# Kernel optimization log

Measured on AMD Instinct MI355X. Metric: run time of the kernel, lower is better.

## Reference

```python
import jax, jax.numpy as jnp
import numpy as np

B, S, D = 64, 196, 768           # batch, num_tokens, dim
E, K = 4, 2                      # num experts (MoM internal default), top-k routing
TH = int(S * 1.0)                # token-mixing hidden (hidden_ratio=1.0)
MH = int(D * 4.0)                # channel MLP hidden (mlp_ratio=4.0)
EPS = 1e-6


def _ln(x, g, b):
    mu = jnp.mean(x, axis=-1, keepdims=True)
    var = jnp.mean((x - mu) ** 2, axis=-1, keepdims=True)
    return (x - mu) / jnp.sqrt(var + EPS) * g + b


def setup_inputs() -> dict:
    key = jax.random.key(0)
    ks = jax.random.split(key, 8)
    w = lambda k, sh: jax.random.normal(k, sh, dtype=jnp.float32) * 0.02
    return {
        "x": jax.random.normal(ks[0], (B, S, D), dtype=jnp.float32),
        "gamma1": jnp.ones((D,), jnp.float32), "beta1": jnp.zeros((D,), jnp.float32),
        "Wg": w(ks[1], (D, E)), "bg": jnp.zeros((E,), jnp.float32),
        "W1": w(ks[2], (E, S, TH)), "b1": jnp.zeros((E, TH), jnp.float32),
        "W2": w(ks[3], (E, TH, S)), "b2": jnp.zeros((E, S), jnp.float32),
        "gamma2": jnp.ones((D,), jnp.float32), "beta2": jnp.zeros((D,), jnp.float32),
        "Wm1": w(ks[4], (D, MH)), "bm1": jnp.zeros((MH,), jnp.float32),
        "Wm2": w(ks[5], (MH, D)), "bm2": jnp.zeros((D,), jnp.float32),
    }


def reference(x, gamma1, beta1, Wg, bg, W1, b1, W2, b2,
              gamma2, beta2, Wm1, bm1, Wm2, bm2):
    # --- pre-norm 1 + MoM token mixer ---
    normed = _ln(x, gamma1, beta1)                               # [B,S,D]
    logits = jnp.mean(normed, axis=1) @ Wg + bg                  # [B,E] per-sample router
    probs = jax.nn.softmax(logits, axis=-1)
    topv, topi = jax.lax.top_k(probs, K)                         # [B,K]
    topv = topv / jnp.sum(topv, axis=-1, keepdims=True)          # renormalize top-k
    combine = jnp.zeros((B, E), probs.dtype).at[jnp.arange(B)[:, None], topi].set(topv)
    xt = jnp.transpose(normed, (0, 2, 1))                        # [B,D,S] mix over tokens
    h = jax.nn.gelu(jnp.einsum('bds,esh->bedh', xt, W1) + b1[None, :, None, :],
                    approximate=False)                           # [B,E,D,TH]
    o = jnp.einsum('bedh,ehs->beds', h, W2) + b2[None, :, None, :]  # [B,E,D,S]
    mom_out = jnp.einsum('be,beds->bsd', combine, o)             # [B,S,D]
    x1 = x + mom_out
    # --- pre-norm 2 + channel MLP ---
    n2 = _ln(x1, gamma2, beta2)
    mlp = jax.nn.gelu(n2 @ Wm1 + bm1, approximate=False) @ Wm2 + bm2
    out = x1 + mlp
    # --- Switch-style load-balancing aux loss ---
    mask = (combine > 0).astype(probs.dtype)                     # [B,E]
    aux_loss = E * jnp.sum(jnp.mean(mask, axis=0) * jnp.mean(probs, axis=0))
    return out, aux_loss
```

## Files before the change

### kernel.cpp

```cpp
#include <hip/hip_runtime.h>
#include <hip/hip_bf16.h>
#include <math.h>

#define BB 64
#define SS 196
#define DD 768
#define EE 4
#define KKE 2
#define THH 196
#define MHH 3072
#define N1 (BB*SS*DD)
#define MM (BB*SS)
#define PP 256

typedef __bf16 bf16x8 __attribute__((ext_vector_type(8)));
typedef float f32x4 __attribute__((ext_vector_type(4)));

__device__ __forceinline__ float gelu_act(float x){
    float y = 1.5957691216057308f*(x + 0.044715f*x*x*x);
    float e = __expf(y);
    float t = 1.f - 2.f/(e+1.f);
    return 0.5f*x*(1.f+t);
}

__global__ __launch_bounds__(256) void ln_bf16_kernel(const float* __restrict__ x,
                                                      const float* __restrict__ g,
                                                      const float* __restrict__ b,
                                                      __hip_bfloat16* __restrict__ out,
                                                      float* __restrict__ muo,
                                                      float* __restrict__ rso){
    int row = blockIdx.x;
    int tid = threadIdx.x;
    const float* xr = x + (size_t)row * DD;
    float v0 = xr[tid], v1 = xr[tid+256], v2 = xr[tid+512];
    float s = v0+v1+v2, ss = v0*v0+v1*v1+v2*v2;
    __shared__ float sh[10];
    int lane = tid & 63, wid = tid >> 6;
    #pragma unroll
    for (int o=32;o>0;o>>=1){ s += __shfl_down(s,o); ss += __shfl_down(ss,o); }
    if (lane==0){ sh[wid]=s; sh[4+wid]=ss; }
    __syncthreads();
    if (tid==0){
        float S1=sh[0]+sh[1]+sh[2]+sh[3], S2=sh[4]+sh[5]+sh[6]+sh[7];
        float mu = S1/DD; float var = S2/DD - mu*mu;
        float rs = rsqrtf(var + 1e-6f);
        sh[8]=mu; sh[9]=rs;
        muo[row]=mu; rso[row]=rs;
    }
    __syncthreads();
    float mu=sh[8], rs=sh[9];
    __hip_bfloat16* orow = out + (size_t)row*DD;
    orow[tid]     = __float2bfloat16((v0-mu)*rs*g[tid]     + b[tid]);
    orow[tid+256] = __float2bfloat16((v1-mu)*rs*g[tid+256] + b[tid+256]);
    orow[tid+512] = __float2bfloat16((v2-mu)*rs*g[tid+512] + b[tid+512]);
}

__global__ __launch_bounds__(256) void transpose_bf16_kernel(const float* __restrict__ src,
                                                             __hip_bfloat16* __restrict__ dst,
                                                             int R, int C){
    __shared__ float t[32][33];
    int c0 = blockIdx.x*32, r0 = blockIdx.y*32;
    int tx = threadIdx.x & 31, ty = threadIdx.x >> 5;
    #pragma unroll
    for (int rr = ty; rr < 32; rr += 8)
        t[rr][tx] = src[(size_t)(r0+rr)*C + c0 + tx];
    __syncthreads();
    #pragma unroll
    for (int cc = ty; cc < 32; cc += 8)
        dst[(size_t)(c0+cc)*R + r0 + tx] = __float2bfloat16(t[tx][cc]);
}

__global__ __launch_bounds__(256) void transpose_pad_w_kernel(const float* __restrict__ src0,
                                                              __hip_bfloat16* __restrict__ dst0,
                                                              int R, int C){
    const float* src = src0 + (size_t)blockIdx.z*R*C;
    __hip_bfloat16* dst = dst0 + (size_t)blockIdx.z*PP*PP;
    __shared__ float t[32][33];
    int c0 = blockIdx.x*32, r0 = blockIdx.y*32;
    int tx = threadIdx.x & 31, ty = threadIdx.x >> 5;
    #pragma unroll
    for (int rr = ty; rr < 32; rr += 8)
        t[rr][tx] = (r0+rr < R && c0+tx < C) ? src[(size_t)(r0+rr)*C + c0 + tx] : 0.f;
    __syncthreads();
    #pragma unroll
    for (int cc = ty; cc < 32; cc += 8)
        dst[(size_t)(c0+cc)*PP + r0 + tx] = __float2bfloat16(t[tx][cc]);
}

__global__ __launch_bounds__(256) void transpose_pad_n_kernel(const __hip_bfloat16* __restrict__ src,
                                                              __hip_bfloat16* __restrict__ dst){
    int b = blockIdx.z;
    __shared__ __hip_bfloat16 t[64][66];
    int d0 = blockIdx.x*64, s0 = blockIdx.y*64;
    int lane = threadIdx.x & 63, q = threadIdx.x >> 6;
    for (int i=q; i<64; i+=4){
        int s = s0+i;
        t[i][lane] = (s < SS) ? src[((size_t)b*SS + s)*DD + d0 + lane]
                              : __float2bfloat16(0.f);
    }
    __syncthreads();
    for (int i=q; i<64; i+=4){
        int d = d0+i;
        dst[((size_t)b*DD + d)*PP + s0 + lane] = t[lane][i];
    }
}

__global__ __launch_bounds__(384) void meanvec_kernel(const float* __restrict__ x,
                                                      const float* __restrict__ mu,
                                                      const float* __restrict__ rs,
                                                      const float* __restrict__ g1,
                                                      const float* __restrict__ b1,
                                                      float* __restrict__ mv){
    int b = blockIdx.y, d = blockIdx.x*384 + threadIdx.x;
    __shared__ float smu[SS], srs[SS];
    for (int s=threadIdx.x; s<SS; s+=384){ smu[s]=mu[b*SS+s]; srs[s]=rs[b*SS+s]; }
    __syncthreads();
    const float* base = x + (size_t)b*SS*DD + d;
    float a0=0.f, a1=0.f;
    for (int s=0;s<SS;s+=2){
        a0 += (base[(size_t)s*DD]     - smu[s])  * srs[s];
        a1 += (base[(size_t)(s+1)*DD] - smu[s+1])* srs[s+1];
    }
    mv[(size_t)b*DD + d] = g1[d]*((a0+a1)/(float)SS) + b1[d];
}

__global__ __launch_bounds__(64) void logits_kernel(const float* __restrict__ mv,
                                                    const float* __restrict__ Wg,
                                                    const float* __restrict__ bg,
                                                    float* __restrict__ combine,
                                                    float* __restrict__ probs,
                                                    int* __restrict__ topi,
                                                    float* __restrict__ topw){
    int b = blockIdx.x, lane = threadIdx.x;
    float pl[EE] = {0.f,0.f,0.f,0.f};
    #pragma unroll
    for (int i=0;i<DD/64;++i){
        int d = lane + i*64;
        float m = mv[(size_t)b*DD + d];
        #pragma unroll
        for (int e=0;e<EE;++e) pl[e] += m * Wg[d*EE + e];
    }
    #pragma unroll
    for (int e=0;e<EE;++e){
        #pragma unroll
        for (int o=32;o>0;o>>=1) pl[e] += __shfl_down(pl[e], o);
    }
    if (lane==0){
        float lg[EE];
        for (int e=0;e<EE;++e) lg[e] = pl[e] + bg[e];
        float mx = lg[0];
        for (int e=1;e<EE;++e) mx = fmaxf(mx, lg[e]);
        float p[EE]; float sum=0.f;
        for (int e=0;e<EE;++e){ p[e]=expf(lg[e]-mx); sum+=p[e]; }
        for (int e=0;e<EE;++e) p[e] /= sum;
        int i0=0; for (int e=1;e<EE;++e) if (p[e]>p[i0]) i0=e;
        int i1=-1;
        for (int e=0;e<EE;++e){ if (e==i0) continue; if (i1<0 || p[e]>p[i1]) i1=e; }
        float v0=p[i0], v1=p[i1], rsum=v0+v1;
        float w0=v0/rsum, w1=v1/rsum;
        for (int e=0;e<EE;++e){ probs[b*EE+e]=p[e]; combine[b*EE+e]=0.f; }
        combine[b*EE+i0]=w0; combine[b*EE+i1]=w1;
        topi[b*KKE]=i0; topi[b*KKE+1]=i1;
        topw[b*KKE]=w0; topw[b*KKE+1]=w1;
    }
}

__global__ __launch_bounds__(256) void aux_kernel(const float* __restrict__ combine,
                                                  const float* __restrict__ probs,
                                                  float* __restrict__ aux_out){
    int tid = threadIdx.x; int e = tid>>6, b = tid&63;
    float m = combine[b*EE+e] > 0.f ? 1.f : 0.f;
    float p = probs[b*EE+e];
    #pragma unroll
    for (int o=32;o>0;o>>=1){ m += __shfl_down(m,o); p += __shfl_down(p,o); }
    __shared__ float sh[EE];
    if ((tid&63)==0) sh[e] = (m/(float)BB)*(p/(float)BB);
    __syncthreads();
    if (tid==0) aux_out[0] = (float)EE * (sh[0]+sh[1]+sh[2]+sh[3]);
}

__global__ __launch_bounds__(256) void tok_gemm1_kernel(
    const __hip_bfloat16* __restrict__ nTp,
    const __hip_bfloat16* __restrict__ w1tp,
    const float* __restrict__ b1,
    const int* __restrict__ topi,
    __hip_bfloat16* __restrict__ htok)
{
    __shared__ __hip_bfloat16 smem[128*64*2];
    __hip_bfloat16* As = smem;
    __hip_bfloat16* Bs = smem + 128*64;
    int tid=threadIdx.x, lane=tid&63, w=tid>>6;
    int wm=w>>1, wn=w&1, l15=lane&15, l4=lane>>4;
    int be = blockIdx.z, b = be>>1;
    int e = __builtin_amdgcn_readfirstlane(topi[b*KKE + (be&1)]);
    int m0 = blockIdx.y*128, n0 = blockIdx.x*128;
    const __hip_bfloat16* A  = nTp  + ((size_t)b*DD + m0)*PP;
    const __hip_bfloat16* Bt = w1tp + ((size_t)e*PP + n0)*PP;
    f32x4 acc[4][4];
    #pragma unroll
    for (int mi=0;mi<4;++mi)
        #pragma unroll
        for (int ni=0;ni<4;++ni) acc[mi][ni] = (f32x4){0.f,0.f,0.f,0.f};

    int srow = w*32 + (lane>>3), sc = lane&7;
    int soff = srow*64 + ((sc ^ (srow&7))<<3);
    const __hip_bfloat16* Ap = A + (size_t)srow*PP + sc*8;
    const __hip_bfloat16* Bp = Bt + (size_t)srow*PP + sc*8;
    bf16x8 va[4], vb[4];
    #pragma unroll
    for (int i=0;i<4;++i){
        va[i] = *reinterpret_cast<const bf16x8*>(Ap + (size_t)i*8*PP);
        vb[i] = *reinterpret_cast<const bf16x8*>(Bp + (size_t)i*8*PP);
    }
    for (int k0=0; k0<PP; k0+=64){
        __syncthreads();
        #pragma unroll
        for (int i=0;i<4;++i){
            *reinterpret_cast<bf16x8*>(&As[soff + i*8*64]) = va[i];
            *reinterpret_cast<bf16x8*>(&Bs[soff + i*8*64]) = vb[i];
        }
        __syncthreads();
        if (k0+64 < PP){
            #pragma unroll
            for (int i=0;i<4;++i){
                va[i] = *reinterpret_cast<const bf16x8*>(Ap + (size_t)i*8*PP + (k0+64));
                vb[i] = *reinterpret_cast<const bf16x8*>(Bp + (size_t)i*8*PP + (k0+64));
            }
        }
        #pragma unroll
        for (int kk=0;kk<2;++kk){
            bf16x8 af[4], bfr[4];
            #pragma unroll
            for (int mi=0;mi<4;++mi){
                int r = wm*64 + mi*16 + l15, kc = kk*4 + l4;
                af[mi] = *reinterpret_cast<const bf16x8*>(&As[r*64 + ((kc ^ (r&7))<<3)]);
            }
            #pragma unroll
            for (int ni=0;ni<4;++ni){
                int r = wn*64 + ni*16 + l15, kc = kk*4 + l4;
                bfr[ni] = *reinterpret_cast<const bf16x8*>(&Bs[r*64 + ((kc ^ (r&7))<<3)]);
            }
            #pragma unroll
            for (int mi=0;mi<4;++mi)
                #pragma unroll
                for (int ni=0;ni<4;++ni)
                    acc[mi][ni] = __builtin_amdgcn_mfma_f32_16x16x32_bf16(af[mi], bfr[ni], acc[mi][ni], 0, 0, 0);
        }
    }
    __syncthreads();
    __hip_bfloat16* Ht = smem;
    #pragma unroll
    for (int mi=0;mi<4;++mi){
        #pragma unroll
        for (int ni=0;ni<4;++ni){
            int colL = wn*64 + ni*16 + l15;
            int col = n0 + colL;
            float bv = (col < THH) ? b1[e*THH + col] : 0.f;
            #pragma unroll
            for (int r=0;r<4;++r){
                int rowL = wm*64 + mi*16 + l4*4 + r;
                float v = (col < THH) ? gelu_act(acc[mi][ni][r] + bv) : 0.f;
                Ht[rowL*128 + colL] = __float2bfloat16(v);
            }
        }
    }
    __syncthreads();
    for (int i = tid; i < 128*128/8; i += 256){
        int rowL = i >> 4, c8 = i & 15;
        *reinterpret_cast<bf16x8*>(&htok[((size_t)be*DD + m0 + rowL)*PP + n0 + c8*8])
            = *reinterpret_cast<const bf16x8*>(&Ht[rowL*128 + c8*8]);
    }
}

__global__ __launch_bounds__(256) void tok_gemm2_kernel(
    const __hip_bfloat16* __restrict__ htok,
    const __hip_bfloat16* __restrict__ w2tp,
    const float* __restrict__ b2,
    const int* __restrict__ topi, const float* __restrict__ topw,
    const float* __restrict__ x, float* __restrict__ x1)
{
    __shared__ __hip_bfloat16 As[128*64];
    __shared__ __hip_bfloat16 Bs[128*64];
    int tid=threadIdx.x, lane=tid&63, w=tid>>6;
    int wm=w>>1, wn=w&1, l15=lane&15, l4=lane>>4;
    int b = blockIdx.z;
    int m0 = blockIdx.y*128, n0 = blockIdx.x*128;
    float w0 = topw[b*KKE], w1 = topw[b*KKE+1];
    f32x4 acc[4][4];
    #pragma unroll
    for (int mi=0;mi<4;++mi)
        #pragma unroll
        for (int ni=0;ni<4;++ni) acc[mi][ni] = (f32x4){0.f,0.f,0.f,0.f};

    int srow = w*32 + (lane>>3), sc = lane&7;
    int soff = srow*64 + ((sc ^ (srow&7))<<3);

    for (int pass=0; pass<2; ++pass){
        int e = __builtin_amdgcn_readfirstlane(topi[b*KKE + pass]);
        const __hip_bfloat16* Ap = htok + ((size_t)(b*KKE+pass)*DD + m0 + srow)*PP + sc*8;
        const __hip_bfloat16* Bp = w2tp + ((size_t)e*PP + n0 + srow)*PP + sc*8;
        bf16x8 va[4], vb[4];
        #pragma unroll
        for (int i=0;i<4;++i){
            va[i] = *reinterpret_cast<const bf16x8*>(Ap + (size_t)i*8*PP);
            vb[i] = *reinterpret_cast<const bf16x8*>(Bp + (size_t)i*8*PP);
        }
        for (int k0=0; k0<PP; k0+=64){
            __syncthreads();
            #pragma unroll
            for (int i=0;i<4;++i){
                *reinterpret_cast<bf16x8*>(&As[soff + i*8*64]) = va[i];
                *reinterpret_cast<bf16x8*>(&Bs[soff + i*8*64]) = vb[i];
            }
            __syncthreads();
            if (k0+64 < PP){
                #pragma unroll
                for (int i=0;i<4;++i){
                    va[i] = *reinterpret_cast<const bf16x8*>(Ap + (size_t)i*8*PP + (k0+64));
                    vb[i] = *reinterpret_cast<const bf16x8*>(Bp + (size_t)i*8*PP + (k0+64));
                }
            }
            #pragma unroll
            for (int kk=0;kk<2;++kk){
                bf16x8 af[4], bfr[4];
                #pragma unroll
                for (int mi=0;mi<4;++mi){
                    int r = wm*64 + mi*16 + l15, kc = kk*4 + l4;
                    af[mi] = *reinterpret_cast<const bf16x8*>(&As[r*64 + ((kc ^ (r&7))<<3)]);
                }
                #pragma unroll
                for (int ni=0;ni<4;++ni){
                    int r = wn*64 + ni*16 + l15, kc = kk*4 + l4;
                    bfr[ni] = *reinterpret_cast<const bf16x8*>(&Bs[r*64 + ((kc ^ (r&7))<<3)]);
                }
                #pragma unroll
                for (int mi=0;mi<4;++mi)
                    #pragma unroll
                    for (int ni=0;ni<4;++ni)
                        acc[mi][ni] = __builtin_amdgcn_mfma_f32_16x16x32_bf16(af[mi], bfr[ni], acc[mi][ni], 0, 0, 0);
            }
        }
        if (pass==0){
            float sc0 = w0 / w1;
            #pragma unroll
            for (int mi=0;mi<4;++mi)
                #pragma unroll
                for (int ni=0;ni<4;++ni)
                    #pragma unroll
                    for (int r=0;r<4;++r) acc[mi][ni][r] *= sc0;
        }
    }
    int e0 = topi[b*KKE], e1 = topi[b*KKE+1];
    #pragma unroll
    for (int mi=0;mi<4;++mi){
        #pragma unroll
        for (int ni=0;ni<4;++ni){
            int col = n0 + wn*64 + ni*16 + l15;
            if (col < SS){
                float bias = w0*b2[e0*SS+col] + w1*b2[e1*SS+col];
                int rowb = m0 + wm*64 + mi*16 + l4*4;
                size_t idx = ((size_t)b*SS + col)*DD + rowb;
                f32x4 xv = *reinterpret_cast<const f32x4*>(x + idx);
                f32x4 res;
                #pragma unroll
                for (int r=0;r<4;++r) res[r] = xv[r] + w1*acc[mi][ni][r] + bias;
                *reinterpret_cast<f32x4*>(x1 + idx) = res;
            }
        }
    }
}

__global__ __launch_bounds__(256) void tokenmix2_kernel(
    const __hip_bfloat16* __restrict__ nbf, const float* __restrict__ x,
    const float* __restrict__ W1, const float* __restrict__ b1,
    const float* __restrict__ W2, const float* __restrict__ b2,
    const int* __restrict__ topi, const float* __restrict__ topw,
    float* __restrict__ x1)
{
    __shared__ __hip_bfloat16 xs[SS][64];
    __shared__ __hip_bfloat16 Hs[THH][64];
    int b = blockIdx.y, d0 = blockIdx.x*64;
    int tid = threadIdx.x, lane = tid&63, w = tid>>6;
    for (int s = w; s < SS; s += 4)
        xs[s][lane] = nbf[((size_t)b*SS + s)*DD + d0 + lane];
    #pragma unroll
    for (int k=0;k<KKE;++k){
        int e = __builtin_amdgcn_readfirstlane(topi[b*KKE+k]);
        float wgt = topw[b*KKE+k];
        __syncthreads();
        const float* W1e = W1 + (size_t)e*SS*THH;
        for (int hj=0; hj<13; ++hj){
            int hb = w + 16*hj;
            if (hj < 12){
                float a0=b1[e*THH+hb], a1=b1[e*THH+hb+4], a2=b1[e*THH+hb+8], a3=b1[e*THH+hb+12];
                for (int s=0;s<SS;++s){
                    float xv = __bfloat162float(xs[s][lane]);
                    const float* wr = W1e + (size_t)s*THH + hb;
                    a0 += xv*wr[0]; a1 += xv*wr[4]; a2 += xv*wr[8]; a3 += xv*wr[12];
                }
                Hs[hb][lane]    = __float2bfloat16(gelu_act(a0));
                Hs[hb+4][lane]  = __float2bfloat16(gelu_act(a1));
                Hs[hb+8][lane]  = __float2bfloat16(gelu_act(a2));
                Hs[hb+12][lane] = __float2bfloat16(gelu_act(a3));
            } else {
                float a0=b1[e*THH+hb];
                for (int s=0;s<SS;++s)
                    a0 += __bfloat162float(xs[s][lane]) * W1e[(size_t)s*THH + hb];
                Hs[hb][lane] = __float2bfloat16(gelu_act(a0));
            }
        }
        __syncthreads();
        const float* W2e = W2 + (size_t)e*THH*SS;
        for (int sj=0; sj<13; ++sj){
            int sb = w + 16*sj;
            if (sj < 12){
                float o0=b2[e*SS+sb], o1=b2[e*SS+sb+4], o2=b2[e*SS+sb+8], o3=b2[e*SS+sb+12];
                for (int h=0;h<THH;++h){
                    float hv = __bfloat162float(Hs[h][lane]);
                    const float* wr = W2e + (size_t)h*SS + sb;
                    o0 += hv*wr[0]; o1 += hv*wr[4]; o2 += hv*wr[8]; o3 += hv*wr[12];
                }
                float ov[4] = {o0,o1,o2,o3};
                #pragma unroll
                for (int u=0;u<4;++u){
                    size_t idx = ((size_t)b*SS + sb + 4*u)*DD + d0 + lane;
                    float val = wgt*ov[u];
                    if (k==0) x1[idx] = x[idx] + val; else x1[idx] += val;
                }
            } else {
                float o0=b2[e*SS+sb];
                for (int h=0;h<THH;++h)
                    o0 += __bfloat162float(Hs[h][lane]) * W2e[(size_t)h*SS + sb];
                size_t idx = ((size_t)b*SS + sb)*DD + d0 + lane;
                float val = wgt*o0;
                if (k==0) x1[idx] = x[idx] + val; else x1[idx] += val;
            }
        }
    }
}

template<int KDIM, int EPI, int BN, int NBLK, int MB>
__global__ __launch_bounds__(256) void gemm_bt_kernel(
    const __hip_bfloat16* __restrict__ A,
    const __hip_bfloat16* __restrict__ Bt,
    const float* __restrict__ bias,
    __hip_bfloat16* __restrict__ Hout,
    float* __restrict__ Cio,
    int Ntot)
{
    constexpr int NFR = BN/32;
    constexpr int BCH = BN/32;
    int id = blockIdx.x;
    int r8 = id & 7, t = id >> 3;
    int qm = t / NBLK, n = t - qm*NBLK;
    int m  = qm*8 + r8;
    if (m >= MB) return;
    int m0 = m*128, n0 = n*BN;

    __shared__ __hip_bfloat16 smem[128*64 + BN*64];
    __hip_bfloat16* As = smem;
    __hip_bfloat16* Bs = smem + 128*64;
    int tid = threadIdx.x, lane = tid&63, w = tid>>6;
    int wm = w>>1, wn = w&1;
    int l15 = lane&15, l4 = lane>>4;
    f32x4 acc[4][NFR];
    #pragma unroll
    for (int mi=0;mi<4;++mi)
        #pragma unroll
        for (int ni=0;ni<NFR;++ni) acc[mi][ni] = (f32x4){0.f,0.f,0.f,0.f};

    int r0 = tid>>3;
    int sc = tid&7;
    int soff = r0*64 + ((sc ^ (r0&7))<<3);
    const __hip_bfloat16* Ap = A  + (size_t)(m0+r0)*KDIM + sc*8;
    const __hip_bfloat16* Bp = Bt + (size_t)(n0+r0)*KDIM + sc*8;

    bf16x8 va[4], vb[BCH];
    #pragma unroll
    for (int i=0;i<4;++i)
        va[i] = *reinterpret_cast<const bf16x8*>(Ap + (size_t)i*32*KDIM);
    #pragma unroll
    for (int i=0;i<BCH;++i)
        vb[i] = *reinterpret_cast<const bf16x8*>(Bp + (size_t)i*32*KDIM);

    for (int k0=0; k0<KDIM; k0+=64){
        __syncthreads();
        #pragma unroll
        for (int i=0;i<4;++i)
            *reinterpret_cast<bf16x8*>(&As[soff + i*32*64]) = va[i];
        #pragma unroll
        for (int i=0;i<BCH;++i)
            *reinterpret_cast<bf16x8*>(&Bs[soff + i*32*64]) = vb[i];
        __syncthreads();
        if (k0+64 < KDIM){
            #pragma unroll
            for (int i=0;i<4;++i)
                va[i] = *reinterpret_cast<const bf16x8*>(Ap + (size_t)i*32*KDIM + (k0+64));
            #pragma unroll
            for (int i=0;i<BCH;++i)
                vb[i] = *reinterpret_cast<const bf16x8*>(Bp + (size_t)i*32*KDIM + (k0+64));
        }
        #pragma unroll
        for (int kk=0;kk<2;++kk){
            bf16x8 af[4], bfr[NFR];
            #pragma unroll
            for (int mi=0;mi<4;++mi){
                int r = wm*64 + mi*16 + l15;
                int kc = kk*4 + l4;
                af[mi] = *reinterpret_cast<const bf16x8*>(&As[r*64 + ((kc ^ (r&7))<<3)]);
            }
            #pragma unroll
            for (int ni=0;ni<NFR;++ni){
                int r = wn*(BN/2) + ni*16 + l15;
                int kc = kk*4 + l4;
                bfr[ni] = *reinterpret_cast<const bf16x8*>(&Bs[r*64 + ((kc ^ (r&7))<<3)]);
            }
            #pragma unroll
            for (int mi=0;mi<4;++mi)
                #pragma unroll
                for (int ni=0;ni<NFR;++ni)
                    acc[mi][ni] = __builtin_amdgcn_mfma_f32_16x16x32_bf16(af[mi], bfr[ni], acc[mi][ni], 0, 0, 0);
        }
    }
    if (EPI==0){
        __syncthreads();
        __hip_bfloat16* Ht = smem;
        #pragma unroll
        for (int mi=0;mi<4;++mi){
            #pragma unroll
            for (int ni=0;ni<NFR;++ni){
                int colL = wn*(BN/2) + ni*16 + l15;
                float bv = bias[n0 + colL];
                #pragma unroll
                for (int r=0;r<4;++r){
                    int rowL = wm*64 + mi*16 + l4*4 + r;
                    Ht[rowL*BN + colL] = __float2bfloat16(gelu_act(acc[mi][ni][r] + bv));
                }
            }
        }
        __syncthreads();
        for (int i = tid; i < 128*BN/8; i += 256){
            int rowL = i / (BN/8), c8 = i % (BN/8);
            *reinterpret_cast<bf16x8*>(&Hout[(size_t)(m0+rowL)*Ntot + n0 + c8*8])
                = *reinterpret_cast<const bf16x8*>(&Ht[rowL*BN + c8*8]);
        }
    } else {
        #pragma unroll
        for (int mi=0;mi<4;++mi){
            #pragma unroll
            for (int ni=0;ni<NFR;++ni){
                int col = n0 + wn*(BN/2) + ni*16 + l15;
                float bv = bias[col];
                #pragma unroll
                for (int r=0;r<4;++r){
                    int row = m0 + wm*64 + mi*16 + l4*4 + r;
                    Cio[(size_t)row*Ntot + col] += acc[mi][ni][r] + bv;
                }
            }
        }
    }
}

__global__ __launch_bounds__(512, 4) void mlp_mfma_kernel(
    const __hip_bfloat16* __restrict__ n2b,
    const __hip_bfloat16* __restrict__ w1t,
    const float* __restrict__ bm1,
    const __hip_bfloat16* __restrict__ w2t,
    const float* __restrict__ bm2,
    float* __restrict__ io)
{
    __shared__ __align__(16) __hip_bfloat16 Ht[32*64];
    int tid = threadIdx.x;
    int wid = tid >> 6, lane = tid & 63;
    int wm = wid >> 2, wn = wid & 3;
    int l15 = lane & 15, l4 = lane >> 4;
    int m0 = blockIdx.x * 32;
    f32x4 acc[12];
    #pragma unroll
    for (int f=0; f<12; ++f) acc[f] = (f32x4){0.f,0.f,0.f,0.f};
    const __hip_bfloat16* aptr = n2b + (size_t)(m0 + wm*16 + l15)*DD + l4*8;
    for (int hc = 0; hc < MHH; hc += 64) {
        f32x4 h = (f32x4){0.f,0.f,0.f,0.f};
        const __hip_bfloat16* bptr = w1t + (size_t)(hc + wn*16 + l15)*DD + l4*8;
        #pragma unroll 4
        for (int ks = 0; ks < DD; ks += 32) {
            bf16x8 a = *reinterpret_cast<const bf16x8*>(aptr + ks);
            bf16x8 bb = *reinterpret_cast<const bf16x8*>(bptr + ks);
            h = __builtin_amdgcn_mfma_f32_16x16x32_bf16(a, bb, h, 0, 0, 0);
        }
        float bv = bm1[hc + wn*16 + l15];
        __syncthreads();
        {
            int col = wn*16 + l15;
            int chunk = col >> 3, inner = col & 7;
            #pragma unroll
            for (int r=0; r<4; ++r) {
                int row = wm*16 + l4*4 + r;
                float v = gelu_act(h[r] + bv);
                Ht[row*64 + ((chunk ^ (row&7))<<3) + inner] = __float2bfloat16(v);
            }
        }
        __syncthreads();
        #pragma unroll
        for (int kk = 0; kk < 2; ++kk) {
            int arow = wm*16 + l15;
            int ach = (kk*32 + l4*8) >> 3;
            bf16x8 aH = *reinterpret_cast<const bf16x8*>(&Ht[arow*64 + ((ach ^ (arow&7))<<3)]);
            const __hip_bfloat16* b2p = w2t + (size_t)(wn*192 + l15)*MHH + hc + kk*32 + l4*8;
            #pragma unroll
            for (int f=0; f<12; ++f) {
                bf16x8 bb = *reinterpret_cast<const bf16x8*>(b2p + (size_t)f*16*MHH);
                acc[f] = __builtin_amdgcn_mfma_f32_16x16x32_bf16(aH, bb, acc[f], 0, 0, 0);
            }
        }
    }
    #pragma unroll
    for (int f=0; f<12; ++f) {
        int col = wn*192 + f*16 + l15;
        float b2v = bm2[col];
        #pragma unroll
        for (int r=0; r<4; ++r) {
            size_t idx = (size_t)(m0 + wm*16 + l4*4 + r)*DD + col;
            io[idx] += acc[f][r] + b2v;
        }
    }
}

extern "C" void kernel_launch(void* const* d_in, const int* in_sizes, int n_in,
                              void* d_out, int out_size, void* d_ws, size_t ws_size,
                              hipStream_t stream) {
    const float* x    = (const float*)d_in[0];
    const float* g1   = (const float*)d_in[1];
    const float* be1  = (const float*)d_in[2];
    const float* Wg   = (const float*)d_in[3];
    const float* bg   = (const float*)d_in[4];
    const float* W1   = (const float*)d_in[5];
    const float* b1e  = (const float*)d_in[6];
    const float* W2   = (const float*)d_in[7];
    const float* b2e  = (const float*)d_in[8];
    const float* g2   = (const float*)d_in[9];
    const float* be2  = (const float*)d_in[10];
    const float* Wm1  = (const float*)d_in[11];
    const float* bm1  = (const float*)d_in[12];
    const float* Wm2  = (const float*)d_in[13];
    const float* bm2  = (const float*)d_in[14];

    float* out = (float*)d_out;
    char* w = (char*)d_ws;

    const size_t OFF_W1T  = 19267584;
    const size_t OFF_W2T  = OFF_W1T + 4718592;
    const size_t OFF_W1TP = OFF_W2T + 4718592;
    const size_t OFF_W2TP = OFF_W1TP + (size_t)EE*PP*PP*2;
    const size_t OFF_REG  = OFF_W2TP + (size_t)EE*PP*PP*2;
    const size_t NTP_B    = (size_t)BB*DD*PP*2;
    const size_t HTOK_B   = (size_t)BB*KKE*DD*PP*2;
    const size_t HMLP_B   = (size_t)MM*MHH*2;
    const size_t REG_B    = (NTP_B + HTOK_B > HMLP_B) ? (NTP_B + HTOK_B) : HMLP_B;
    const size_t REG_END  = OFF_REG + REG_B;
    const size_t NEED     = REG_END + 400000;
    bool bigws = (ws_size >= NEED);

    __hip_bfloat16* nbf  = (__hip_bfloat16*)w;
    __hip_bfloat16* w1t  = (__hip_bfloat16*)(w + OFF_W1T);
    __hip_bfloat16* w2t  = (__hip_bfloat16*)(w + OFF_W2T);
    __hip_bfloat16* w1tp = (__hip_bfloat16*)(w + OFF_W1TP);
    __hip_bfloat16* w2tp = (__hip_bfloat16*)(w + OFF_W2TP);
    __hip_bfloat16* nTp  = (__hip_bfloat16*)(w + OFF_REG);
    __hip_bfloat16* htok = (__hip_bfloat16*)(w + OFF_REG + NTP_B);
    __hip_bfloat16* Hmlp = (__hip_bfloat16*)(w + OFF_REG);

    size_t tail = bigws ? REG_END : OFF_W1TP;
    float* muv     = (float*)(w + tail);
    float* rsigv   = muv + MM;
    float* mv      = rsigv + MM;
    float* combine = mv + (size_t)BB*DD;
    float* probs   = combine + BB*EE;
    float* topw    = probs + BB*EE;
    int*   topi    = (int*)(topw + BB*KKE);

    transpose_bf16_kernel<<<dim3(MHH/32, DD/32), 256, 0, stream>>>(Wm1, w1t, DD, MHH);
    transpose_bf16_kernel<<<dim3(DD/32, MHH/32), 256, 0, stream>>>(Wm2, w2t, MHH, DD);
    if (bigws){
        transpose_pad_w_kernel<<<dim3(PP/32, PP/32, EE), 256, 0, stream>>>(W1, w1tp, SS, THH);
        transpose_pad_w_kernel<<<dim3(PP/32, PP/32, EE), 256, 0, stream>>>(W2, w2tp, THH, SS);
    }
    ln_bf16_kernel<<<MM, 256, 0, stream>>>(x, g1, be1, nbf, muv, rsigv);
    meanvec_kernel<<<dim3(2, BB), 384, 0, stream>>>(x, muv, rsigv, g1, be1, mv);
    logits_kernel<<<BB, 64, 0, stream>>>(mv, Wg, bg, combine, probs, topi, topw);
    aux_kernel<<<1, 256, 0, stream>>>(combine, probs, out + N1);
    if (bigws){
        transpose_pad_n_kernel<<<dim3(DD/64, PP/64, BB), 256, 0, stream>>>(nbf, nTp);
        tok_gemm1_kernel<<<dim3(PP/128, DD/128, BB*KKE), 256, 0, stream>>>(nTp, w1tp, b1e, topi, htok);
        tok_gemm2_kernel<<<dim3(PP/128, DD/128, BB), 256, 0, stream>>>(htok, w2tp, b2e, topi, topw, x, out);
    } else {
        tokenmix2_kernel<<<dim3(DD/64, BB), 256, 0, stream>>>(nbf, x, W1, b1e, W2, b2e,
                                                              topi, topw, out);
    }
    ln_bf16_kernel<<<MM, 256, 0, stream>>>(out, g2, be2, nbf, muv, rsigv);
    if (bigws){
        gemm_bt_kernel<DD, 0, 128, MHH/128, MM/128><<<8*13*(MHH/128), 256, 0, stream>>>(
            nbf, w1t, bm1, Hmlp, nullptr, MHH);
        gemm_bt_kernel<MHH, 1, 64, DD/64, MM/128><<<8*13*(DD/64), 256, 0, stream>>>(
            Hmlp, w2t, bm2, nullptr, out, DD);
    } else {
        mlp_mfma_kernel<<<MM/32, 512, 0, stream>>>(nbf, w1t, bm1, w2t, bm2, out);
    }
}
```

Before: 344.1 us.

## Double-buffer second MLP GEMM with direct global-to-LDS async loads

Splits the templated GEMM into a GELU-epilogue kernel for the first MLP projection and a new kernel for the second projection. The new kernel uses global_load_lds to copy tiles straight into a double-buffered, XOR-swizzled shared memory layout, overlapping the next K-tile load with MFMA on the current one and needing only one barrier per iteration. This targets the register-staged load and store and the extra syncs in the long K=3072 loop. It doubles LDS use, which may lower occupancy.

```diff
diff --git a/kernel.cpp b/kernel.cpp
--- a/kernel.cpp
+++ b/kernel.cpp
@@ -22,6 +22,10 @@
     float t = 1.f - 2.f/(e+1.f);
     return 0.5f*x*(1.f+t);
 }
+
+#define GLD16(ldsp, gp) \
+    __builtin_amdgcn_global_load_lds((__attribute__((address_space(1))) void*)(gp), \
+                                     (__attribute__((address_space(3))) void*)(ldsp), 16, 0, 0)
 
 __global__ __launch_bounds__(256) void ln_bf16_kernel(const float* __restrict__ x,
                                                       const float* __restrict__ g,
@@ -439,17 +443,15 @@
     }
 }
 
-template<int KDIM, int EPI, int BN, int NBLK, int MB>
+template<int KDIM, int NBLK, int MB>
 __global__ __launch_bounds__(256) void gemm_bt_kernel(
     const __hip_bfloat16* __restrict__ A,
     const __hip_bfloat16* __restrict__ Bt,
     const float* __restrict__ bias,
     __hip_bfloat16* __restrict__ Hout,
-    float* __restrict__ Cio,
     int Ntot)
 {
-    constexpr int NFR = BN/32;
-    constexpr int BCH = BN/32;
+    constexpr int BN = 128;
     int id = blockIdx.x;
     int r8 = id & 7, t = id >> 3;
     int qm = t / NBLK, n = t - qm*NBLK;
@@ -463,11 +465,11 @@
     int tid = threadIdx.x, lane = tid&63, w = tid>>6;
     int wm = w>>1, wn = w&1;
     int l15 = lane&15, l4 = lane>>4;
-    f32x4 acc[4][NFR];
+    f32x4 acc[4][4];
     #pragma unroll
     for (int mi=0;mi<4;++mi)
         #pragma unroll
-        for (int ni=0;ni<NFR;++ni) acc[mi][ni] = (f32x4){0.f,0.f,0.f,0.f};
+        for (int ni=0;ni<4;++ni) acc[mi][ni] = (f32x4){0.f,0.f,0.f,0.f};
 
     int r0 = tid>>3;
     int sc = tid&7;
@@ -475,34 +477,30 @@
     const __hip_bfloat16* Ap = A  + (size_t)(m0+r0)*KDIM + sc*8;
     const __hip_bfloat16* Bp = Bt + (size_t)(n0+r0)*KDIM + sc*8;
 
-    bf16x8 va[4], vb[BCH];
-    #pragma unroll
-    for (int i=0;i<4;++i)
+    bf16x8 va[4], vb[4];
+    #pragma unroll
+    for (int i=0;i<4;++i){
         va[i] = *reinterpret_cast<const bf16x8*>(Ap + (size_t)i*32*KDIM);
-    #pragma unroll
-    for (int i=0;i<BCH;++i)
         vb[i] = *reinterpret_cast<const bf16x8*>(Bp + (size_t)i*32*KDIM);
-
+    }
     for (int k0=0; k0<KDIM; k0+=64){
         __syncthreads();
         #pragma unroll
-        for (int i=0;i<4;++i)
+        for (int i=0;i<4;++i){
             *reinterpret_cast<bf16x8*>(&As[soff + i*32*64]) = va[i];
-        #pragma unroll
-        for (int i=0;i<BCH;++i)
             *reinterpret_cast<bf16x8*>(&Bs[soff + i*32*64]) = vb[i];
+        }
         __syncthreads();
         if (k0+64 < KDIM){
             #pragma unroll
-            for (int i=0;i<4;++i)
+            for (int i=0;i<4;++i){
                 va[i] = *reinterpret_cast<const bf16x8*>(Ap + (size_t)i*32*KDIM + (k0+64));
-            #pragma unroll
-            for (int i=0;i<BCH;++i)
                 vb[i] = *reinterpret_cast<const bf16x8*>(Bp + (size_t)i*32*KDIM + (k0+64));
+            }
         }
         #pragma unroll
         for (int kk=0;kk<2;++kk){
-            bf16x8 af[4], bfr[NFR];
+            bf16x8 af[4], bfr[4];
             #pragma unroll
             for (int mi=0;mi<4;++mi){
                 int r = wm*64 + mi*16 + l15;
@@ -510,52 +508,127 @@
                 af[mi] = *reinterpret_cast<const bf16x8*>(&As[r*64 + ((kc ^ (r&7))<<3)]);
             }
             #pragma unroll
-            for (int ni=0;ni<NFR;++ni){
-                int r = wn*(BN/2) + ni*16 + l15;
+            for (int ni=0;ni<4;++ni){
+                int r = wn*64 + ni*16 + l15;
                 int kc = kk*4 + l4;
                 bfr[ni] = *reinterpret_cast<const bf16x8*>(&Bs[r*64 + ((kc ^ (r&7))<<3)]);
             }
             #pragma unroll
             for (int mi=0;mi<4;++mi)
                 #pragma unroll
-                for (int ni=0;ni<NFR;++ni)
+                for (int ni=0;ni<4;++ni)
                     acc[mi][ni] = __builtin_amdgcn_mfma_f32_16x16x32_bf16(af[mi], bfr[ni], acc[mi][ni], 0, 0, 0);
         }
     }
-    if (EPI==0){
-        __syncthreads();
-        __hip_bfloat16* Ht = smem;
-        #pragma unroll
-        for (int mi=0;mi<4;++mi){
-            #pragma unroll
-            for (int ni=0;ni<NFR;++ni){
-                int colL = wn*(BN/2) + ni*16 + l15;
-                float bv = bias[n0 + colL];
-                #pragma unroll
-                for (int r=0;r<4;++r){
-                    int rowL = wm*64 + mi*16 + l4*4 + r;
-                    Ht[rowL*BN + colL] = __float2bfloat16(gelu_act(acc[mi][ni][r] + bv));
-                }
-            }
-        }
-        __syncthreads();
-        for (int i = tid; i < 128*BN/8; i += 256){
-            int rowL = i / (BN/8), c8 = i % (BN/8);
-            *reinterpret_cast<bf16x8*>(&Hout[(size_t)(m0+rowL)*Ntot + n0 + c8*8])
-                = *reinterpret_cast<const bf16x8*>(&Ht[rowL*BN + c8*8]);
-        }
-    } else {
-        #pragma unroll
-        for (int mi=0;mi<4;++mi){
-            #pragma unroll
-            for (int ni=0;ni<NFR;++ni){
-                int col = n0 + wn*(BN/2) + ni*16 + l15;
-                float bv = bias[col];
-                #pragma unroll
-                for (int r=0;r<4;++r){
-                    int row = m0 + wm*64 + mi*16 + l4*4 + r;
-                    Cio[(size_t)row*Ntot + col] += acc[mi][ni][r] + bv;
-                }
+    __syncthreads();
+    __hip_bfloat16* Ht = smem;
+    #pragma unroll
+    for (int mi=0;mi<4;++mi){
+        #pragma unroll
+        for (int ni=0;ni<4;++ni){
+            int colL = wn*64 + ni*16 + l15;
+            float bv = bias[n0 + colL];
+            #pragma unroll
+            for (int r=0;r<4;++r){
+                int rowL = wm*64 + mi*16 + l4*4 + r;
+                Ht[rowL*BN + colL] = __float2bfloat16(gelu_act(acc[mi][ni][r] + bv));
+            }
+        }
+    }
+    __syncthreads();
+    for (int i = tid; i < 128*BN/8; i += 256){
+        int rowL = i / (BN/8), c8 = i % (BN/8);
+        *reinterpret_cast<bf16x8*>(&Hout[(size_t)(m0+rowL)*Ntot + n0 + c8*8])
+            = *reinterpret_cast<const bf16x8*>(&Ht[rowL*BN + c8*8]);
+    }
+}
+
+template<int KDIM, int NBLK, int MB>
+__global__ __launch_bounds__(256) void gemm2_pipe_kernel(
+    const __hip_bfloat16* __restrict__ A,
+    const __hip_bfloat16* __restrict__ Bt,
+    const float* __restrict__ bias,
+    float* __restrict__ Cio,
+    int Ntot)
+{
+    constexpr int BN = 64;
+    int id = blockIdx.x;
+    int r8 = id & 7, t = id >> 3;
+    int qm = t / NBLK, n = t - qm*NBLK;
+    int m  = qm*8 + r8;
+    if (m >= MB) return;
+    int m0 = m*128, n0 = n*BN;
+
+    __shared__ __hip_bfloat16 As[2][128*64];
+    __shared__ __hip_bfloat16 Bs[2][BN*64];
+    int tid = threadIdx.x, lane = tid&63, w = tid>>6;
+    int wm = w>>1, wn = w&1;
+    int l15 = lane&15, l4 = lane>>4;
+    f32x4 acc[4][2];
+    #pragma unroll
+    for (int mi=0;mi<4;++mi){ acc[mi][0]=(f32x4){0,0,0,0}; acc[mi][1]=(f32x4){0,0,0,0}; }
+
+    const __hip_bfloat16* Ag = A  + (size_t)m0*KDIM;
+    const __hip_bfloat16* Bg = Bt + (size_t)n0*KDIM;
+
+    auto stage = [&](int p, int k0){
+        #pragma unroll
+        for (int i=0;i<4;++i){
+            int cb = i*256 + w*64;
+            int cg = cb + lane;
+            int row = cg>>3;
+            int col = ((cg&7) ^ (row&7))*8;
+            GLD16(&As[p][cb*8], Ag + (size_t)row*KDIM + k0 + col);
+        }
+        #pragma unroll
+        for (int i=0;i<2;++i){
+            int cb = i*256 + w*64;
+            int cg = cb + lane;
+            int row = cg>>3;
+            int col = ((cg&7) ^ (row&7))*8;
+            GLD16(&Bs[p][cb*8], Bg + (size_t)row*KDIM + k0 + col);
+        }
+    };
+
+    stage(0, 0);
+    __syncthreads();
+    int cur = 0;
+    for (int k0=0; k0<KDIM; k0+=64){
+        if (k0+64 < KDIM) stage(cur^1, k0+64);
+        #pragma unroll
+        for (int kk=0;kk<2;++kk){
+            bf16x8 af[4], bfr[2];
+            #pragma unroll
+            for (int mi=0;mi<4;++mi){
+                int r = wm*64 + mi*16 + l15;
+                int kc = kk*4 + l4;
+                af[mi] = *reinterpret_cast<const bf16x8*>(&As[cur][r*64 + ((kc ^ (r&7))<<3)]);
+            }
+            #pragma unroll
+            for (int ni=0;ni<2;++ni){
+                int r = wn*32 + ni*16 + l15;
+                int kc = kk*4 + l4;
+                bfr[ni] = *reinterpret_cast<const bf16x8*>(&Bs[cur][r*64 + ((kc ^ (r&7))<<3)]);
+            }
+            #pragma unroll
+            for (int mi=0;mi<4;++mi){
+                acc[mi][0] = __builtin_amdgcn_mfma_f32_16x16x32_bf16(af[mi], bfr[0], acc[mi][0], 0, 0, 0);
+                acc[mi][1] = __builtin_amdgcn_mfma_f32_16x16x32_bf16(af[mi], bfr[1], acc[mi][1], 0, 0, 0);
+            }
+        }
+        __syncthreads();
+        cur ^= 1;
+    }
+    #pragma unroll
+    for (int mi=0;mi<4;++mi){
+        #pragma unroll
+        for (int ni=0;ni<2;++ni){
+            int col = n0 + wn*32 + ni*16 + l15;
+            float bv = bias[col];
+            #pragma unroll
+            for (int r=0;r<4;++r){
+                int row = m0 + wm*64 + mi*16 + l4*4 + r;
+                Cio[(size_t)row*Ntot + col] += acc[mi][ni][r] + bv;
             }
         }
     }
@@ -699,10 +772,10 @@
     }
     ln_bf16_kernel<<<MM, 256, 0, stream>>>(out, g2, be2, nbf, muv, rsigv);
     if (bigws){
-        gemm_bt_kernel<DD, 0, 128, MHH/128, MM/128><<<8*13*(MHH/128), 256, 0, stream>>>(
-            nbf, w1t, bm1, Hmlp, nullptr, MHH);
-        gemm_bt_kernel<MHH, 1, 64, DD/64, MM/128><<<8*13*(DD/64), 256, 0, stream>>>(
-            Hmlp, w2t, bm2, nullptr, out, DD);
+        gemm_bt_kernel<DD, MHH/128, MM/128><<<8*13*(MHH/128), 256, 0, stream>>>(
+            nbf, w1t, bm1, Hmlp, MHH);
+        gemm2_pipe_kernel<MHH, DD/64, MM/128><<<8*13*(DD/64), 256, 0, stream>>>(
+            Hmlp, w2t, bm2, out, DD);
     } else {
         mlp_mfma_kernel<<<MM/32, 512, 0, stream>>>(nbf, w1t, bm1, w2t, bm2, out);
     }
```

Result: slower. 351.1 us (+2.0%).
